# Optimization experiments

Hardware: AMD Instinct MI355X
Metric: run time of the kernel (lower is better)

Reference implementation:

```python
import jax, jax.numpy as jnp
import numpy as np

N_NODES = 100000
N_EDGES = 1600000
D_IN = 64
D_OUT = 64


def setup_inputs() -> dict:
    key = jax.random.key(0)
    k1, k2, k3, k4, k5, k6 = jax.random.split(key, 6)
    x = jax.random.normal(k1, (N_NODES, D_IN), dtype=jnp.float32)
    edge_index = jax.random.randint(k2, (2, N_EDGES), 0, N_NODES, dtype=jnp.int64)
    edge_weight = jax.random.uniform(k3, (N_EDGES,), dtype=jnp.float32)
    scale = 1.0 / np.sqrt(D_IN)
    W0 = jax.random.normal(k4, (D_IN, D_OUT), dtype=jnp.float32) * scale
    W1 = jax.random.normal(k5, (D_IN, D_OUT), dtype=jnp.float32) * scale
    b = jax.random.normal(k6, (D_OUT,), dtype=jnp.float32) * 0.01
    return {"x": x, "edge_index": edge_index, "edge_weight": edge_weight,
            "W0": W0, "W1": W1, "b": b}


def reference(x, edge_index, edge_weight, W0, W1, b):
    # ChebConv K=2 with default lambda_max=2.0, sym normalization:
    # L_hat = 2L/lambda_max - I = -D^{-1/2} A D^{-1/2}
    N = x.shape[0]
    row, col = edge_index[0], edge_index[1]
    deg = jax.ops.segment_sum(edge_weight, row, num_segments=N)  # [N]
    deg_safe = jnp.where(deg > 0, deg, 1.0)
    dinv = jnp.where(deg > 0, jax.lax.rsqrt(deg_safe), 0.0)
    norm = -dinv[row] * edge_weight * dinv[col]  # [E], L_hat edge weights
    # Tx_1[i] = sum_{e: col_e = i} norm_e * x[row_e]
    Tx1 = jax.ops.segment_sum(norm[:, None] * x[row], col, num_segments=N)
    # out = lin0(Tx_0) + lin1(Tx_1) + bias
    return x @ W0 + Tx1 @ W1 + b
```

## Files before the change

### kernel.cpp

```cpp
#include <hip/hip_runtime.h>

#define N_NODES 100000
#define N_EDGES 1600000
#define D 64
#define NC 391
#define NCP 392
#define NBLK 256
#define EPB 6250
#define CAPC 5120
#define AST 68

__device__ __forceinline__ unsigned bf16rne(float f) {
    unsigned u = __float_as_uint(f);
    return (u + 0x7FFFu + ((u >> 16) & 1u)) >> 16;
}
__global__ __launch_bounds__(256) void tobf16_kernel(const float* __restrict__ x,
                                                     ushort* __restrict__ xh,
                                                     float* __restrict__ deg4,
                                                     int* __restrict__ btot) {
    int id = blockIdx.x * 256 + threadIdx.x;
    if (id < 4 * N_NODES) deg4[id] = 0.f;
    if (id < NC) btot[id] = 0;
    int i = id * 8;
    float4 a = *(const float4*)(x + i);
    float4 b = *(const float4*)(x + i + 4);
    uint4 o;
    o.x = bf16rne(a.x) | (bf16rne(a.y) << 16);
    o.y = bf16rne(a.z) | (bf16rne(a.w) << 16);
    o.z = bf16rne(b.x) | (bf16rne(b.y) << 16);
    o.w = bf16rne(b.z) | (bf16rne(b.w) << 16);
    *(uint4*)(xh + i) = o;
}

__global__ __launch_bounds__(512) void countdeg_kernel(const int* __restrict__ row,
                                                       const int* __restrict__ col,
                                                       const float* __restrict__ w,
                                                       float* __restrict__ deg4,
                                                       int* __restrict__ cntT,
                                                       int* __restrict__ btot) {
    __shared__ int h[NCP];
    int t = threadIdx.x;
    int b = blockIdx.x;
    for (int j = t; j < NCP; j += 512) h[j] = 0;
    __syncthreads();
    int base = b * EPB;
    float* dg = deg4 + (size_t)(b & 3) * N_NODES;
    for (int i = t; i < EPB; i += 512) {
        int e = base + i;
        atomicAdd(&dg[row[e]], w[e]);
        atomicAdd(&h[col[e] >> 8], 1);
    }
    __syncthreads();
    for (int j = t; j < NC; j += 512) {
        int v = h[j];
        cntT[(size_t)j * NBLK + b] = v;
        if (v) atomicAdd(&btot[j], v);
    }
}

__global__ __launch_bounds__(512) void scanD_kernel(const int* __restrict__ btot,
                                                    int* __restrict__ cbase,
                                                    int* __restrict__ cntT,
                                                    const float* __restrict__ deg4,
                                                    float* __restrict__ dinv) {
    __shared__ int sc[512];
    __shared__ int wsum[8];
    int j = blockIdx.x;
    int t = threadIdx.x;
    int bt = (t < NC) ? btot[t] : 0;
    sc[t] = bt;
    __syncthreads();
    for (int off = 1; off < 512; off <<= 1) {
        int u = (t >= off) ? sc[t - off] : 0;
        __syncthreads();
        sc[t] += u;
        __syncthreads();
    }
    int cbv = sc[j] - btot[j];
    if (t == 0) cbase[j] = cbv;
    if (j == 0 && t == 0) cbase[NC] = N_EDGES;
    int v = (t < NBLK) ? cntT[(size_t)j * NBLK + t] : 0;
    int lane = t & 63, wv = t >> 6;
    int inc = v;
    #pragma unroll
    for (int d = 1; d < 64; d <<= 1) {
        int u = __shfl_up(inc, d, 64);
        if (lane >= d) inc += u;
    }
    if (lane == 63) wsum[wv] = inc;
    __syncthreads();
    int woff = 0;
    for (int w2 = 0; w2 < wv; ++w2) woff += wsum[w2];
    if (t < NBLK) cntT[(size_t)j * NBLK + t] = cbv + woff + inc - v;
    if (t < 256) {
        int n = j * 256 + t;
        if (n < N_NODES) {
            float d = deg4[n] + deg4[N_NODES + n] + deg4[2 * N_NODES + n]
                    + deg4[3 * N_NODES + n];
            dinv[n] = d > 0.f ? rsqrtf(d) : 0.f;
        }
    }
}

__global__ __launch_bounds__(512) void scatterA_kernel(const int* __restrict__ row,
                                                       const int* __restrict__ col,
                                                       const float* __restrict__ w,
                                                       const int* __restrict__ cntT,
                                                       int2* __restrict__ recA) {
    __shared__ int curs[NCP];
    int t = threadIdx.x;
    int b = blockIdx.x;
    for (int j = t; j < NC; j += 512) curs[j] = cntT[(size_t)j * NBLK + b];
    __syncthreads();
    int base = b * EPB;
    for (int i = t; i < EPB; i += 512) {
        int e = base + i;
        int r = row[e];
        int c = col[e];
        float we = w[e];
        int p = atomicAdd(&curs[c >> 8], 1);
        recA[p] = make_int2(((c & 255) << 17) | r, __float_as_int(we));
    }
}

__global__ __launch_bounds__(256) void sortB_kernel(const int* __restrict__ cbase,
                                                    const float* __restrict__ dinv,
                                                    int2* __restrict__ recA,
                                                    int* __restrict__ node_start) {
    __shared__ int2 buf[CAPC];
    __shared__ int h[256];
    __shared__ int cu[256];
    __shared__ int wsum[4];
    int t = threadIdx.x;
    int cb = blockIdx.x;
    int base = cbase[cb];
    int cnt = min(cbase[cb + 1] - base, CAPC);
    h[t] = 0;
    __syncthreads();
    for (int i = t; i < cnt; i += 256)
        atomicAdd(&h[(recA[base + i].x >> 17) & 255], 1);
    __syncthreads();
    int v = h[t];
    int lane = t & 63, wv = t >> 6;
    int inc = v;
    #pragma unroll
    for (int d2 = 1; d2 < 64; d2 <<= 1) {
        int u = __shfl_up(inc, d2, 64);
        if (lane >= d2) inc += u;
    }
    if (lane == 63) wsum[wv] = inc;
    __syncthreads();
    int woff = 0;
    for (int w2 = 0; w2 < wv; ++w2) woff += wsum[w2];
    int st = woff + inc - v;
    cu[t] = st;
    int nid = cb * 256 + t;
    if (nid <= N_NODES) node_start[nid] = base + st;
    __syncthreads();
    for (int i = t; i < cnt; i += 256) {
        int2 rc = recA[base + i];
        int r = rc.x & 0x1FFFF;
        float cf = __int_as_float(rc.y) * dinv[r];
        int p = atomicAdd(&cu[(rc.x >> 17) & 255], 1);
        buf[p] = make_int2(r, __float_as_int(cf));
    }
    __syncthreads();
    for (int i = t; i < cnt; i += 256) recA[base + i] = buf[i];
}

#define FMA_BF16T(e, u, A, B)                                                  \
    do { float cc = __int_as_float((e).y);                                     \
        A.x += cc * __uint_as_float((u).x << 16);                              \
        A.y += cc * __uint_as_float((u).x & 0xFFFF0000u);                      \
        A.z += cc * __uint_as_float((u).y << 16);                              \
        A.w += cc * __uint_as_float((u).y & 0xFFFF0000u);                      \
        B.x += cc * __uint_as_float((u).z << 16);                              \
        B.y += cc * __uint_as_float((u).z & 0xFFFF0000u);                      \
        B.z += cc * __uint_as_float((u).w << 16);                              \
        B.w += cc * __uint_as_float((u).w & 0xFFFF0000u);                      \
    } while (0)

__global__ __launch_bounds__(256, 8) void gather_out_kernel(
        const int2* __restrict__ recS, const int* __restrict__ node_start,
        const float* __restrict__ dinv, const ushort* __restrict__ xh,
        const float* __restrict__ x, const float* __restrict__ W0,
        const float* __restrict__ W1, const float* __restrict__ bias,
        float* __restrict__ out) {
    __shared__ __align__(16) float xs[32 * AST];
    __shared__ __align__(16) float ts[32 * AST];
    __shared__ int s33[33];

    int tid = threadIdx.x;
    int b   = blockIdx.x;
    int n0  = b * 32;
    int g   = tid >> 3;
    int j   = tid & 7;

    if (tid < 33) s33[tid] = node_start[n0 + tid];
    __syncthreads();
    int ks = s33[g];
    int ke = s33[g + 1];

    float4 p0 = make_float4(0.f, 0.f, 0.f, 0.f);
    float4 p1 = make_float4(0.f, 0.f, 0.f, 0.f);
    float4 q0 = make_float4(0.f, 0.f, 0.f, 0.f);
    float4 q1 = make_float4(0.f, 0.f, 0.f, 0.f);
    const ushort* xhj = xh + (j << 3);

    int k = ks;
    for (; k + 3 < ke; k += 4) {
        int2 e0 = recS[k + 0];
        int2 e1 = recS[k + 1];
        int2 e2 = recS[k + 2];
        int2 e3 = recS[k + 3];
        uint4 u0 = *(const uint4*)(xhj + ((size_t)e0.x << 6));
        uint4 u1 = *(const uint4*)(xhj + ((size_t)e1.x << 6));
        uint4 u2 = *(const uint4*)(xhj + ((size_t)e2.x << 6));
        uint4 u3 = *(const uint4*)(xhj + ((size_t)e3.x << 6));
        FMA_BF16T(e0, u0, p0, p1);
        FMA_BF16T(e1, u1, q0, q1);
        FMA_BF16T(e2, u2, p0, p1);
        FMA_BF16T(e3, u3, q0, q1);
    }
    for (; k < ke; ++k) {
        int2 e0 = recS[k];
        uint4 u0 = *(const uint4*)(xhj + ((size_t)e0.x << 6));
        FMA_BF16T(e0, u0, p0, p1);
    }
    float4 acc0 = make_float4(p0.x + q0.x, p0.y + q0.y, p0.z + q0.z, p0.w + q0.w);
    float4 acc1 = make_float4(p1.x + q1.x, p1.y + q1.y, p1.z + q1.z, p1.w + q1.w);

    float dn = -dinv[n0 + g];
    float* tp = ts + g * AST + (j << 3);
    *(float4*)tp       = make_float4(dn * acc0.x, dn * acc0.y, dn * acc0.z, dn * acc0.w);
    *(float4*)(tp + 4) = make_float4(dn * acc1.x, dn * acc1.y, dn * acc1.z, dn * acc1.w);
    for (int i = tid; i < 512; i += 256) {
        int nn = i >> 4;
        int kk = (i & 15) << 2;
        *(float4*)&xs[nn * AST + kk] = *(const float4*)(x + (size_t)n0 * D + i * 4);
    }
    __syncthreads();

    int jl = j << 3;
    float4 o0 = *(const float4*)(bias + jl);
    float4 o1 = *(const float4*)(bias + jl + 4);
    for (int k2 = 0; k2 < D; k2 += 4) {
        float4 av = *(const float4*)&xs[g * AST + k2];
        float4 tv = *(const float4*)&ts[g * AST + k2];
        #pragma unroll
        for (int u = 0; u < 4; ++u) {
            float a = (u == 0) ? av.x : (u == 1) ? av.y : (u == 2) ? av.z : av.w;
            float t = (u == 0) ? tv.x : (u == 1) ? tv.y : (u == 2) ? tv.z : tv.w;
            const float4 w00 = *(const float4*)(W0 + (size_t)(k2 + u) * D + jl);
            const float4 w01 = *(const float4*)(W0 + (size_t)(k2 + u) * D + jl + 4);
            const float4 w10 = *(const float4*)(W1 + (size_t)(k2 + u) * D + jl);
            const float4 w11 = *(const float4*)(W1 + (size_t)(k2 + u) * D + jl + 4);
            o0.x += a * w00.x + t * w10.x;
            o0.y += a * w00.y + t * w10.y;
            o0.z += a * w00.z + t * w10.z;
            o0.w += a * w00.w + t * w10.w;
            o1.x += a * w01.x + t * w11.x;
            o1.y += a * w01.y + t * w11.y;
            o1.z += a * w01.z + t * w11.z;
            o1.w += a * w01.w + t * w11.w;
        }
    }
    float* op = out + (size_t)(n0 + g) * D + jl;
    *(float4*)op       = o0;
    *(float4*)(op + 4) = o1;
}

extern "C" void kernel_launch(void* const* d_in, const int* in_sizes, int n_in,
                              void* d_out, int out_size, void* d_ws, size_t ws_size,
                              hipStream_t stream) {
    const float* x    = (const float*)d_in[0];
    const int*   eidx = (const int*)d_in[1];
    const float* ew   = (const float*)d_in[2];
    const float* W0   = (const float*)d_in[3];
    const float* W1   = (const float*)d_in[4];
    const float* b    = (const float*)d_in[5];
    float* out = (float*)d_out;

    const int* row = eidx;
    const int* col = eidx + N_EDGES;

    int2*   recA  = (int2*)d_ws;
    int*    cntT  = (int*)(recA + N_EDGES);
    int*    btot  = cntT + (size_t)NC * NBLK;
    int*    cbase = btot + 400;
    float*  deg4  = (float*)(cbase + 400);
    float*  dinv  = deg4 + 4 * N_NODES;
    int*    node_start = (int*)(dinv + N_NODES);
    ushort* xh    = (ushort*)(node_start + 100016);

    tobf16_kernel   <<<N_NODES * D / (256 * 8), 256, 0, stream>>>(x, xh, deg4, btot);
    countdeg_kernel <<<NBLK, 512, 0, stream>>>(row, col, ew, deg4, cntT, btot);
    scanD_kernel    <<<NC, 512, 0, stream>>>(btot, cbase, cntT, deg4, dinv);
    scatterA_kernel <<<NBLK, 512, 0, stream>>>(row, col, ew, cntT, recA);
    sortB_kernel    <<<NC, 256, 0, stream>>>(cbase, dinv, recA, node_start);
    gather_out_kernel<<<N_NODES / 32, 256, 0, stream>>>(recA, node_start, dinv,
                                                        xh, x, W0, W1, b, out);
}
```

Measured before the change: 343.9 us.

## Fuse per-node sort into gather kernel using 32-node buckets

Changes the counting sort from 256-node coarse buckets plus a separate sortB pass to 32-node buckets matching the gather block. The fine-grained per-node sort now happens in shared memory inside the gather kernel, and the dinv[row] scaling moves into the scatter pass. This removes one full read/write pass over the edge records and the node_start array. In exchange it adds a single-block serial scan kernel, more histogram buckets per block with fewer scatter blocks, and more syncs inside the gather loop.

```diff
diff --git a/kernel.cpp b/kernel.cpp
--- a/kernel.cpp
+++ b/kernel.cpp
@@ -3,11 +3,11 @@
 #define N_NODES 100000
 #define N_EDGES 1600000
 #define D 64
-#define NC 391
-#define NCP 392
-#define NBLK 256
-#define EPB 6250
-#define CAPC 5120
+#define NBUCK 3125
+#define NBP 3136
+#define NBLK 128
+#define EPB 12500
+#define CAP 1024
 #define AST 68
 
 __device__ __forceinline__ unsigned bf16rne(float f) {
@@ -20,7 +20,7 @@
                                                      int* __restrict__ btot) {
     int id = blockIdx.x * 256 + threadIdx.x;
     if (id < 4 * N_NODES) deg4[id] = 0.f;
-    if (id < NC) btot[id] = 0;
+    if (id < NBUCK) btot[id] = 0;
     int i = id * 8;
     float4 a = *(const float4*)(x + i);
     float4 b = *(const float4*)(x + i + 4);
@@ -36,159 +36,130 @@
                                                        const int* __restrict__ col,
                                                        const float* __restrict__ w,
                                                        float* __restrict__ deg4,
-                                                       int* __restrict__ cntT,
+                                                       int* __restrict__ cntM,
                                                        int* __restrict__ btot) {
-    __shared__ int h[NCP];
+    __shared__ int h[NBP];
     int t = threadIdx.x;
     int b = blockIdx.x;
-    for (int j = t; j < NCP; j += 512) h[j] = 0;
+    for (int j = t; j < NBP; j += 512) h[j] = 0;
     __syncthreads();
     int base = b * EPB;
     float* dg = deg4 + (size_t)(b & 3) * N_NODES;
     for (int i = t; i < EPB; i += 512) {
         int e = base + i;
         atomicAdd(&dg[row[e]], w[e]);
-        atomicAdd(&h[col[e] >> 8], 1);
-    }
-    __syncthreads();
-    for (int j = t; j < NC; j += 512) {
+        atomicAdd(&h[col[e] >> 5], 1);
+    }
+    __syncthreads();
+    int* mc = cntM + (size_t)b * NBP;
+    for (int j = t; j < NBUCK; j += 512) {
         int v = h[j];
-        cntT[(size_t)j * NBLK + b] = v;
+        mc[j] = v;
         if (v) atomicAdd(&btot[j], v);
     }
 }
 
-__global__ __launch_bounds__(512) void scanD_kernel(const int* __restrict__ btot,
-                                                    int* __restrict__ cbase,
-                                                    int* __restrict__ cntT,
+__global__ __launch_bounds__(512) void scanTot_kernel(const int* __restrict__ btot,
+                                                      int* __restrict__ cbase) {
+    __shared__ int sc[512];
+    int t = threadIdx.x;
+    int carry = 0;
+    for (int c0 = 0; c0 < NBUCK; c0 += 512) {
+        int idx = c0 + t;
+        int v = (idx < NBUCK) ? btot[idx] : 0;
+        sc[t] = v;
+        __syncthreads();
+        for (int off = 1; off < 512; off <<= 1) {
+            int u = (t >= off) ? sc[t - off] : 0;
+            __syncthreads();
+            sc[t] += u;
+            __syncthreads();
+        }
+        if (idx < NBUCK) cbase[idx] = carry + sc[t] - v;
+        int top = sc[511];
+        __syncthreads();
+        carry += top;
+    }
+    if (t == 0) cbase[NBUCK] = N_EDGES;
+}
+
+__global__ __launch_bounds__(128) void scanD_kernel(const int* __restrict__ cbase,
+                                                    int* __restrict__ cntM,
                                                     const float* __restrict__ deg4,
                                                     float* __restrict__ dinv) {
-    __shared__ int sc[512];
-    __shared__ int wsum[8];
+    __shared__ int w0tot;
     int j = blockIdx.x;
     int t = threadIdx.x;
-    int bt = (t < NC) ? btot[t] : 0;
-    sc[t] = bt;
-    __syncthreads();
-    for (int off = 1; off < 512; off <<= 1) {
-        int u = (t >= off) ? sc[t - off] : 0;
-        __syncthreads();
-        sc[t] += u;
-        __syncthreads();
-    }
-    int cbv = sc[j] - btot[j];
-    if (t == 0) cbase[j] = cbv;
-    if (j == 0 && t == 0) cbase[NC] = N_EDGES;
-    int v = (t < NBLK) ? cntT[(size_t)j * NBLK + t] : 0;
-    int lane = t & 63, wv = t >> 6;
+    int v = cntM[(size_t)t * NBP + j];
+    int lane = t & 63;
     int inc = v;
     #pragma unroll
     for (int d = 1; d < 64; d <<= 1) {
         int u = __shfl_up(inc, d, 64);
         if (lane >= d) inc += u;
     }
-    if (lane == 63) wsum[wv] = inc;
-    __syncthreads();
-    int woff = 0;
-    for (int w2 = 0; w2 < wv; ++w2) woff += wsum[w2];
-    if (t < NBLK) cntT[(size_t)j * NBLK + t] = cbv + woff + inc - v;
-    if (t < 256) {
-        int n = j * 256 + t;
-        if (n < N_NODES) {
-            float d = deg4[n] + deg4[N_NODES + n] + deg4[2 * N_NODES + n]
-                    + deg4[3 * N_NODES + n];
-            dinv[n] = d > 0.f ? rsqrtf(d) : 0.f;
-        }
+    if (t == 63) w0tot = inc;
+    __syncthreads();
+    int off = (t >= 64) ? w0tot : 0;
+    cntM[(size_t)t * NBP + j] = cbase[j] + off + inc - v;
+    if (t < 32) {
+        int n = j * 32 + t;
+        float d = deg4[n] + deg4[N_NODES + n] + deg4[2 * N_NODES + n]
+                + deg4[3 * N_NODES + n];
+        dinv[n] = d > 0.f ? rsqrtf(d) : 0.f;
     }
 }
 
 __global__ __launch_bounds__(512) void scatterA_kernel(const int* __restrict__ row,
                                                        const int* __restrict__ col,
                                                        const float* __restrict__ w,
-                                                       const int* __restrict__ cntT,
+                                                       const float* __restrict__ dinv,
+                                                       const int* __restrict__ cntM,
                                                        int2* __restrict__ recA) {
-    __shared__ int curs[NCP];
+    __shared__ int curs[NBP];
     int t = threadIdx.x;
     int b = blockIdx.x;
-    for (int j = t; j < NC; j += 512) curs[j] = cntT[(size_t)j * NBLK + b];
+    const int* mc = cntM + (size_t)b * NBP;
+    for (int j = t; j < NBUCK; j += 512) curs[j] = mc[j];
     __syncthreads();
     int base = b * EPB;
     for (int i = t; i < EPB; i += 512) {
         int e = base + i;
         int r = row[e];
         int c = col[e];
-        float we = w[e];
-        int p = atomicAdd(&curs[c >> 8], 1);
-        recA[p] = make_int2(((c & 255) << 17) | r, __float_as_int(we));
-    }
-}
-
-__global__ __launch_bounds__(256) void sortB_kernel(const int* __restrict__ cbase,
-                                                    const float* __restrict__ dinv,
-                                                    int2* __restrict__ recA,
-                                                    int* __restrict__ node_start) {
-    __shared__ int2 buf[CAPC];
-    __shared__ int h[256];
-    __shared__ int cu[256];
-    __shared__ int wsum[4];
-    int t = threadIdx.x;
-    int cb = blockIdx.x;
-    int base = cbase[cb];
-    int cnt = min(cbase[cb + 1] - base, CAPC);
-    h[t] = 0;
-    __syncthreads();
-    for (int i = t; i < cnt; i += 256)
-        atomicAdd(&h[(recA[base + i].x >> 17) & 255], 1);
-    __syncthreads();
-    int v = h[t];
-    int lane = t & 63, wv = t >> 6;
-    int inc = v;
-    #pragma unroll
-    for (int d2 = 1; d2 < 64; d2 <<= 1) {
-        int u = __shfl_up(inc, d2, 64);
-        if (lane >= d2) inc += u;
-    }
-    if (lane == 63) wsum[wv] = inc;
-    __syncthreads();
-    int woff = 0;
-    for (int w2 = 0; w2 < wv; ++w2) woff += wsum[w2];
-    int st = woff + inc - v;
-    cu[t] = st;
-    int nid = cb * 256 + t;
-    if (nid <= N_NODES) node_start[nid] = base + st;
-    __syncthreads();
-    for (int i = t; i < cnt; i += 256) {
-        int2 rc = recA[base + i];
-        int r = rc.x & 0x1FFFF;
-        float cf = __int_as_float(rc.y) * dinv[r];
-        int p = atomicAdd(&cu[(rc.x >> 17) & 255], 1);
-        buf[p] = make_int2(r, __float_as_int(cf));
-    }
-    __syncthreads();
-    for (int i = t; i < cnt; i += 256) recA[base + i] = buf[i];
-}
-
-#define FMA_BF16T(e, u, A, B)                                                  \
+        float cf = w[e] * dinv[r];
+        int p = atomicAdd(&curs[c >> 5], 1);
+        recA[p] = make_int2(((c & 31) << 17) | r, __float_as_int(cf));
+    }
+}
+
+#define FMA_BF16(e, u)                                                         \
     do { float cc = __int_as_float((e).y);                                     \
-        A.x += cc * __uint_as_float((u).x << 16);                              \
-        A.y += cc * __uint_as_float((u).x & 0xFFFF0000u);                      \
-        A.z += cc * __uint_as_float((u).y << 16);                              \
-        A.w += cc * __uint_as_float((u).y & 0xFFFF0000u);                      \
-        B.x += cc * __uint_as_float((u).z << 16);                              \
-        B.y += cc * __uint_as_float((u).z & 0xFFFF0000u);                      \
-        B.z += cc * __uint_as_float((u).w << 16);                              \
-        B.w += cc * __uint_as_float((u).w & 0xFFFF0000u);                      \
+        acc0.x += cc * __uint_as_float((u).x << 16);                           \
+        acc0.y += cc * __uint_as_float((u).x & 0xFFFF0000u);                   \
+        acc0.z += cc * __uint_as_float((u).y << 16);                           \
+        acc0.w += cc * __uint_as_float((u).y & 0xFFFF0000u);                   \
+        acc1.x += cc * __uint_as_float((u).z << 16);                           \
+        acc1.y += cc * __uint_as_float((u).z & 0xFFFF0000u);                   \
+        acc1.z += cc * __uint_as_float((u).w << 16);                           \
+        acc1.w += cc * __uint_as_float((u).w & 0xFFFF0000u);                   \
     } while (0)
 
 __global__ __launch_bounds__(256, 8) void gather_out_kernel(
-        const int2* __restrict__ recS, const int* __restrict__ node_start,
+        const int2* __restrict__ recA, const int* __restrict__ cbase,
         const float* __restrict__ dinv, const ushort* __restrict__ xh,
         const float* __restrict__ x, const float* __restrict__ W0,
         const float* __restrict__ W1, const float* __restrict__ bias,
         float* __restrict__ out) {
-    __shared__ __align__(16) float xs[32 * AST];
-    __shared__ __align__(16) float ts[32 * AST];
-    __shared__ int s33[33];
+    __shared__ __align__(16) char smemA[32 * AST * 4];
+    __shared__ __align__(16) char smemB[32 * AST * 4];
+    __shared__ int cnt32[32];
+    __shared__ int start32[32];
+    __shared__ int cur32[32];
+    int2*  srt = (int2*)smemA;
+    float* xs  = (float*)smemA;
+    int2*  stg = (int2*)smemB;
+    float* ts  = (float*)smemB;
 
     int tid = threadIdx.x;
     int b   = blockIdx.x;
@@ -196,39 +167,65 @@
     int g   = tid >> 3;
     int j   = tid & 7;
 
-    if (tid < 33) s33[tid] = node_start[n0 + tid];
-    __syncthreads();
-    int ks = s33[g];
-    int ke = s33[g + 1];
-
-    float4 p0 = make_float4(0.f, 0.f, 0.f, 0.f);
-    float4 p1 = make_float4(0.f, 0.f, 0.f, 0.f);
-    float4 q0 = make_float4(0.f, 0.f, 0.f, 0.f);
-    float4 q1 = make_float4(0.f, 0.f, 0.f, 0.f);
+    int base = cbase[b];
+    int cnt  = cbase[b + 1] - base;
+
+    float4 acc0 = make_float4(0.f, 0.f, 0.f, 0.f);
+    float4 acc1 = make_float4(0.f, 0.f, 0.f, 0.f);
     const ushort* xhj = xh + (j << 3);
 
-    int k = ks;
-    for (; k + 3 < ke; k += 4) {
-        int2 e0 = recS[k + 0];
-        int2 e1 = recS[k + 1];
-        int2 e2 = recS[k + 2];
-        int2 e3 = recS[k + 3];
-        uint4 u0 = *(const uint4*)(xhj + ((size_t)e0.x << 6));
-        uint4 u1 = *(const uint4*)(xhj + ((size_t)e1.x << 6));
-        uint4 u2 = *(const uint4*)(xhj + ((size_t)e2.x << 6));
-        uint4 u3 = *(const uint4*)(xhj + ((size_t)e3.x << 6));
-        FMA_BF16T(e0, u0, p0, p1);
-        FMA_BF16T(e1, u1, q0, q1);
-        FMA_BF16T(e2, u2, p0, p1);
-        FMA_BF16T(e3, u3, q0, q1);
-    }
-    for (; k < ke; ++k) {
-        int2 e0 = recS[k];
-        uint4 u0 = *(const uint4*)(xhj + ((size_t)e0.x << 6));
-        FMA_BF16T(e0, u0, p0, p1);
-    }
-    float4 acc0 = make_float4(p0.x + q0.x, p0.y + q0.y, p0.z + q0.z, p0.w + q0.w);
-    float4 acc1 = make_float4(p1.x + q1.x, p1.y + q1.y, p1.z + q1.z, p1.w + q1.w);
+    for (int cb = 0; cb < cnt; cb += CAP) {
+        int m = min(CAP, cnt - cb);
+        if (tid < 32) cnt32[tid] = 0;
+        __syncthreads();
+        for (int i = tid; i < m; i += 256) {
+            int2 rc = recA[base + cb + i];
+            stg[i] = rc;
+            atomicAdd(&cnt32[(rc.x >> 17) & 31], 1);
+        }
+        __syncthreads();
+        if (tid < 32) {
+            int v = cnt32[tid];
+            int inc = v;
+            #pragma unroll
+            for (int d = 1; d < 32; d <<= 1) {
+                int u = __shfl_up(inc, d, 32);
+                if (tid >= d) inc += u;
+            }
+            start32[tid] = inc - v;
+            cur32[tid]   = inc - v;
+        }
+        __syncthreads();
+        for (int i = tid; i < m; i += 256) {
+            int2 rc = stg[i];
+            int p = atomicAdd(&cur32[(rc.x >> 17) & 31], 1);
+            srt[p] = make_int2(rc.x & 0x1FFFF, rc.y);
+        }
+        __syncthreads();
+        int ks = start32[g];
+        int ke = cur32[g];
+        int k = ks;
+        for (; k + 3 < ke; k += 4) {
+            int2 e0 = srt[k + 0];
+            int2 e1 = srt[k + 1];
+            int2 e2 = srt[k + 2];
+            int2 e3 = srt[k + 3];
+            uint4 u0 = *(const uint4*)(xhj + ((size_t)e0.x << 6));
+            uint4 u1 = *(const uint4*)(xhj + ((size_t)e1.x << 6));
+            uint4 u2 = *(const uint4*)(xhj + ((size_t)e2.x << 6));
+            uint4 u3 = *(const uint4*)(xhj + ((size_t)e3.x << 6));
+            FMA_BF16(e0, u0);
+            FMA_BF16(e1, u1);
+            FMA_BF16(e2, u2);
+            FMA_BF16(e3, u3);
+        }
+        for (; k < ke; ++k) {
+            int2 e0 = srt[k];
+            uint4 u0 = *(const uint4*)(xhj + ((size_t)e0.x << 6));
+            FMA_BF16(e0, u0);
+        }
+        __syncthreads();
+    }
 
     float dn = -dinv[n0 + g];
     float* tp = ts + g * AST + (j << 3);
@@ -285,19 +282,18 @@
     const int* col = eidx + N_EDGES;
 
     int2*   recA  = (int2*)d_ws;
-    int*    cntT  = (int*)(recA + N_EDGES);
-    int*    btot  = cntT + (size_t)NC * NBLK;
-    int*    cbase = btot + 400;
-    float*  deg4  = (float*)(cbase + 400);
+    int*    cntM  = (int*)(recA + N_EDGES);
+    int*    btot  = cntM + (size_t)NBLK * NBP;
+    int*    cbase = btot + 3200;
+    float*  deg4  = (float*)(cbase + 3200);
     float*  dinv  = deg4 + 4 * N_NODES;
-    int*    node_start = (int*)(dinv + N_NODES);
-    ushort* xh    = (ushort*)(node_start + 100016);
+    ushort* xh    = (ushort*)(dinv + N_NODES);
 
     tobf16_kernel   <<<N_NODES * D / (256 * 8), 256, 0, stream>>>(x, xh, deg4, btot);
-    countdeg_kernel <<<NBLK, 512, 0, stream>>>(row, col, ew, deg4, cntT, btot);
-    scanD_kernel    <<<NC, 512, 0, stream>>>(btot, cbase, cntT, deg4, dinv);
-    scatterA_kernel <<<NBLK, 512, 0, stream>>>(row, col, ew, cntT, recA);
-    sortB_kernel    <<<NC, 256, 0, stream>>>(cbase, dinv, recA, node_start);
-    gather_out_kernel<<<N_NODES / 32, 256, 0, stream>>>(recA, node_start, dinv,
-                                                        xh, x, W0, W1, b, out);
-}
+    countdeg_kernel <<<NBLK, 512, 0, stream>>>(row, col, ew, deg4, cntM, btot);
+    scanTot_kernel  <<<1, 512, 0, stream>>>(btot, cbase);
+    scanD_kernel    <<<NBUCK, 128, 0, stream>>>(cbase, cntM, deg4, dinv);
+    scatterA_kernel <<<NBLK, 512, 0, stream>>>(row, col, ew, dinv, cntM, recA);
+    gather_out_kernel<<<NBUCK, 256, 0, stream>>>(recA, cbase, dinv,
+                                                 xh, x, W0, W1, b, out);
+}
```

Measured after the change: 382.8 us. +11.3%, slower.
